# Optimization experiments

Hardware: AMD Instinct MI355X
Metric: run time of the kernel (lower is better)

Reference implementation:

```python
import jax, jax.numpy as jnp
import numpy as np

N_ATOMS, N_NBH, N_IN, N_FILTERS, N_OUT, N_GAUSS = 10000, 48, 128, 128, 128, 25
R_CUTOFF = 5.0
LOG2 = float(np.log(2.0))


def ssp(v):
    # shifted softplus, the SchNet activation
    return jax.nn.softplus(v) - LOG2


def setup_inputs() -> dict:
    key = jax.random.key(0)
    ks = jax.random.split(key, 10)
    x = jax.random.normal(ks[0], (N_ATOMS, N_IN), dtype=jnp.float32)
    dR = jax.random.uniform(ks[1], (N_ATOMS, N_NBH), dtype=jnp.float32) * 10.0  # distances in [0,10)
    dR_expanded = jax.random.normal(ks[2], (N_ATOMS, N_NBH, N_GAUSS), dtype=jnp.float32)
    pairwise_mask = jnp.ones((N_ATOMS, N_NBH), dtype=jnp.float32)
    neighbors_idx = jax.random.randint(ks[3], (N_ATOMS, N_NBH), 0, N_ATOMS, dtype=jnp.int32)
    s = 1.0 / np.sqrt(N_FILTERS)
    W1 = jax.random.normal(ks[4], (N_GAUSS, N_FILTERS), dtype=jnp.float32) * (1.0 / np.sqrt(N_GAUSS))
    b1 = jnp.zeros((N_FILTERS,), dtype=jnp.float32)
    W2 = jax.random.normal(ks[5], (N_FILTERS, N_FILTERS), dtype=jnp.float32) * s
    b2 = jnp.zeros((N_FILTERS,), dtype=jnp.float32)
    W_in2f = jax.random.normal(ks[6], (N_IN, N_FILTERS), dtype=jnp.float32) * (1.0 / np.sqrt(N_IN))
    W_f2out = jax.random.normal(ks[7], (N_FILTERS, N_OUT), dtype=jnp.float32) * s
    b_f2out = jnp.zeros((N_OUT,), dtype=jnp.float32)
    return {"x": x, "dR": dR, "dR_expanded": dR_expanded, "pairwise_mask": pairwise_mask,
            "neighbors_idx": neighbors_idx, "W1": W1, "b1": b1, "W2": W2, "b2": b2,
            "W_in2f": W_in2f, "W_f2out": W_f2out, "b_f2out": b_f2out}


def reference(x, dR, dR_expanded, pairwise_mask, neighbors_idx,
              W1, b1, W2, b2, W_in2f, W_f2out, b_f2out):
    # FilterNetwork: Dense + ssp + Dense, on Gaussian-smeared distances -> [N, K, F]
    W = jnp.einsum('nkg,gf->nkf', dR_expanded, W1) + b1
    W = jnp.einsum('nkf,fh->nkh', ssp(W), W2) + b2
    # HardCutoff: 1 where within cutoff
    C = (dR <= R_CUTOFF).astype(W.dtype)           # [N, K]
    W = W * C[..., None]
    # in2f (no bias), gather neighbor features
    y = x @ W_in2f                                  # [N, F]
    y = jnp.take(y, neighbors_idx, axis=0)          # [N, K, F] (gather == take_along_axis path)
    # filter-weighted multiply + masked sum aggregation over neighbor axis
    y = y * W
    y = jnp.sum(y * pairwise_mask[..., None], axis=1)  # [N, F]
    # f2out: Linear + shifted softplus
    return ssp(y @ W_f2out + b_f2out)               # [N, n_out]
```

## Files before the change

### kernel.cpp

```cpp
#include <hip/hip_runtime.h>
#include <hip/hip_bf16.h>


#define NA 10000
#define NK 48
#define NF 128
#define AT 4
#define DREP 40
#define HP   136

typedef __bf16 bf16x8 __attribute__((ext_vector_type(8)));
typedef float  f32x4  __attribute__((ext_vector_type(4)));

__device__ __forceinline__ unsigned short f2bs(float x) {
    return __builtin_bit_cast(unsigned short, (__bf16)x);
}
__device__ __forceinline__ float bs2f(unsigned short u) {
    return (float)__builtin_bit_cast(__bf16, u);
}
__device__ __forceinline__ float sspf(float v) {
    return fmaxf(v, 0.0f) + __logf(1.0f + __expf(-fabsf(v))) - 0.69314718056f;
}

__global__ __launch_bounds__(256) void prep_weights(
    const float* __restrict__ W1,
    const float* __restrict__ W2,
    const float* __restrict__ Wi,
    unsigned short* __restrict__ wsb)
{
    int i = blockIdx.x * 256 + threadIdx.x;
    if (i < 4096) {
        int f = i >> 5, g = i & 31;
        wsb[i] = (g < 25) ? f2bs(W1[g * NF + f]) : (unsigned short)0;
    } else if (i < 20480) {
        int j = i - 4096; int h = j >> 7, k = j & 127;
        wsb[i] = f2bs(W2[k * NF + h]);
    } else if (i < 36864) {
        int j = i - 20480; int f = j >> 7, k = j & 127;
        wsb[i] = f2bs(Wi[k * NF + f]);
    }
}

__global__ __launch_bounds__(256) void in2f_mfma(
    const float* __restrict__ x,
    const unsigned short* __restrict__ WiT,
    unsigned short* __restrict__ yfeatb)
{
    const int tid = threadIdx.x;
    const int w = tid >> 6;
    const int lane = tid & 63;
    const int r = lane & 15;
    const int q = lane >> 4;
    const int nt0 = w * 2;
    const int m0 = blockIdx.x * 16;

    bf16x8 a[4];
    #pragma unroll
    for (int ks = 0; ks < 4; ++ks) {
        const float4* xp = (const float4*)(x + (size_t)(m0 + r) * NF + ks * 32 + q * 8);
        float4 v0 = xp[0], v1 = xp[1];
        a[ks][0]=(__bf16)v0.x; a[ks][1]=(__bf16)v0.y; a[ks][2]=(__bf16)v0.z; a[ks][3]=(__bf16)v0.w;
        a[ks][4]=(__bf16)v1.x; a[ks][5]=(__bf16)v1.y; a[ks][6]=(__bf16)v1.z; a[ks][7]=(__bf16)v1.w;
    }

    f32x4 acc[2];
    acc[0] = (f32x4){0.f,0.f,0.f,0.f};
    acc[1] = (f32x4){0.f,0.f,0.f,0.f};
    #pragma unroll
    for (int ks = 0; ks < 4; ++ks) {
        bf16x8 b0 = *(const bf16x8*)(WiT + ((nt0    ) * 16 + r) * NF + ks * 32 + q * 8);
        bf16x8 b1 = *(const bf16x8*)(WiT + ((nt0 + 1) * 16 + r) * NF + ks * 32 + q * 8);
        acc[0] = __builtin_amdgcn_mfma_f32_16x16x32_bf16(a[ks], b0, acc[0], 0, 0, 0);
        acc[1] = __builtin_amdgcn_mfma_f32_16x16x32_bf16(a[ks], b1, acc[1], 0, 0, 0);
    }
    #pragma unroll
    for (int t = 0; t < 2; ++t)
        #pragma unroll
        for (int reg = 0; reg < 4; ++reg)
            yfeatb[(size_t)(m0 + q * 4 + reg) * NF + (nt0 + t) * 16 + r] = f2bs(acc[t][reg]);
}

__global__ __launch_bounds__(256) void cfconv_mfma(
    const float* __restrict__ dR,
    const float* __restrict__ dRe,
    const float* __restrict__ mask,
    const int*   __restrict__ nbr,
    const float* __restrict__ b1,
    const float* __restrict__ b2,
    const float* __restrict__ Wf2o,
    const float* __restrict__ bf2o,
    const unsigned short* __restrict__ W1T,
    const unsigned short* __restrict__ W2T,
    const unsigned short* __restrict__ yfeatb,
    float* __restrict__ out)
{
    __shared__ __align__(16) unsigned short s_dre[NK * DREP];
    __shared__ __align__(16) unsigned short s_H[NK * HP];
    __shared__ __align__(16) float s_y4[AT][NF];
    __shared__ __align__(16) float s_part[AT][256];
    __shared__ float s_cm[NK];
    __shared__ int   s_nb[NK];

    const int tid = threadIdx.x;
    const int w = tid >> 6;
    const int lane = tid & 63;
    const int r = lane & 15;
    const int q = lane >> 4;
    const int nt0 = w * 2;
    const int n0 = blockIdx.x * AT;

    const float bias1a = b1[nt0 * 16 + r];
    const float bias1b = b1[nt0 * 16 + 16 + r];
    const float bias2a = b2[nt0 * 16 + r];
    const float bias2b = b2[nt0 * 16 + 16 + r];
    bf16x8 bfr0 = *(const bf16x8*)(W1T + ((nt0    ) * 16 + r) * 32 + q * 8);
    bf16x8 bfr1 = *(const bf16x8*)(W1T + ((nt0 + 1) * 16 + r) * 32 + q * 8);
    bf16x8 bw[2][4];
    #pragma unroll
    for (int t = 0; t < 2; ++t)
        #pragma unroll
        for (int ks = 0; ks < 4; ++ks)
            bw[t][ks] = *(const bf16x8*)(W2T + ((nt0 + t) * 16 + r) * NF + ks * 32 + q * 8);

    {
        unsigned int* z = (unsigned int*)s_dre;
        for (int i = tid; i < NK * DREP / 2; i += 256) z[i] = 0u;
    }
    __syncthreads();

    for (int a = 0; a < AT; ++a) {
        const int n = n0 + a;

        if (tid < NK) {
            float d = dR[n * NK + tid];
            float m = mask[n * NK + tid];
            s_cm[tid] = (d <= 5.0f) ? m : 0.0f;
            s_nb[tid] = nbr[n * NK + tid] * NF;
        }
        {
            const float* dre = dRe + (size_t)n * (NK * 25);
            #pragma unroll
            for (int i = tid; i < NK * 25; i += 256) {
                int k = i / 25;
                int g = i - k * 25;
                s_dre[k * DREP + g] = f2bs(dre[i]);
            }
        }
        __syncthreads();

        #pragma unroll
        for (int mt = 0; mt < 3; ++mt) {
            bf16x8 af = *(const bf16x8*)(&s_dre[(mt * 16 + r) * DREP + q * 8]);
            f32x4 zf = (f32x4){0.f,0.f,0.f,0.f};
            f32x4 h0 = __builtin_amdgcn_mfma_f32_16x16x32_bf16(af, bfr0, zf, 0, 0, 0);
            f32x4 h1 = __builtin_amdgcn_mfma_f32_16x16x32_bf16(af, bfr1, zf, 0, 0, 0);
            #pragma unroll
            for (int reg = 0; reg < 4; ++reg) {
                int k = mt * 16 + q * 4 + reg;
                s_H[k * HP + nt0 * 16 + r]      = f2bs(sspf(h0[reg] + bias1a));
                s_H[k * HP + nt0 * 16 + 16 + r] = f2bs(sspf(h1[reg] + bias1b));
            }
        }
        __syncthreads();

        f32x4 acc[3][2];
        #pragma unroll
        for (int mt = 0; mt < 3; ++mt) {
            acc[mt][0] = (f32x4){0.f,0.f,0.f,0.f};
            acc[mt][1] = (f32x4){0.f,0.f,0.f,0.f};
        }
        #pragma unroll
        for (int ks = 0; ks < 4; ++ks) {
            #pragma unroll
            for (int mt = 0; mt < 3; ++mt) {
                bf16x8 af = *(const bf16x8*)(&s_H[(mt * 16 + r) * HP + ks * 32 + q * 8]);
                acc[mt][0] = __builtin_amdgcn_mfma_f32_16x16x32_bf16(af, bw[0][ks], acc[mt][0], 0, 0, 0);
                acc[mt][1] = __builtin_amdgcn_mfma_f32_16x16x32_bf16(af, bw[1][ks], acc[mt][1], 0, 0, 0);
            }
        }

        float part0 = 0.f, part1 = 0.f;
        const int h0i = nt0 * 16 + r;
        #pragma unroll
        for (int mt = 0; mt < 3; ++mt) {
            #pragma unroll
            for (int reg = 0; reg < 4; ++reg) {
                int k = mt * 16 + q * 4 + reg;
                float cmk = s_cm[k];
                int base = s_nb[k];
                part0 = fmaf(cmk * (acc[mt][0][reg] + bias2a), bs2f(yfeatb[base + h0i]), part0);
                part1 = fmaf(cmk * (acc[mt][1][reg] + bias2b), bs2f(yfeatb[base + h0i + 16]), part1);
            }
        }
        part0 += __shfl_xor(part0, 16);
        part0 += __shfl_xor(part0, 32);
        part1 += __shfl_xor(part1, 16);
        part1 += __shfl_xor(part1, 32);
        if (q == 0) {
            s_y4[a][h0i] = part0;
            s_y4[a][h0i + 16] = part1;
        }
        __syncthreads();
    }

    {
        int f = tid & 127;
        int half = tid >> 7;
        float o0 = 0.f, o1 = 0.f, o2 = 0.f, o3 = 0.f;
        const float* wp = Wf2o + (size_t)(half * 64) * NF + f;
        const float* y0 = &s_y4[0][half * 64];
        const float* y1 = &s_y4[1][half * 64];
        const float* y2 = &s_y4[2][half * 64];
        const float* y3 = &s_y4[3][half * 64];
        #pragma unroll 8
        for (int i = 0; i < 64; ++i) {
            float wv = wp[(size_t)i * NF];
            o0 = fmaf(y0[i], wv, o0);
            o1 = fmaf(y1[i], wv, o1);
            o2 = fmaf(y2[i], wv, o2);
            o3 = fmaf(y3[i], wv, o3);
        }
        s_part[0][tid] = o0;
        s_part[1][tid] = o1;
        s_part[2][tid] = o2;
        s_part[3][tid] = o3;
    }
    __syncthreads();
    if (tid < NF) {
        float bo = bf2o[tid];
        #pragma unroll
        for (int a = 0; a < AT; ++a)
            out[(size_t)(n0 + a) * NF + tid] = sspf(s_part[a][tid] + s_part[a][tid + 128] + bo);
    }
}

extern "C" void kernel_launch(void* const* d_in, const int* in_sizes, int n_in,
                              void* d_out, int out_size, void* d_ws, size_t ws_size,
                              hipStream_t stream)
{
    const float* x    = (const float*)d_in[0];
    const float* dR   = (const float*)d_in[1];
    const float* dRe  = (const float*)d_in[2];
    const float* mask = (const float*)d_in[3];
    const int*   nbr  = (const int*)d_in[4];
    const float* W1   = (const float*)d_in[5];
    const float* b1   = (const float*)d_in[6];
    const float* W2   = (const float*)d_in[7];
    const float* b2   = (const float*)d_in[8];
    const float* Wi2f = (const float*)d_in[9];
    const float* Wf2o = (const float*)d_in[10];
    const float* bf2o = (const float*)d_in[11];
    float* out = (float*)d_out;

    unsigned short* wsb = (unsigned short*)d_ws;
    unsigned short* W1T    = wsb;
    unsigned short* W2T    = wsb + 4096;
    unsigned short* WiT    = wsb + 20480;
    unsigned short* yfeatb = wsb + 36864;

    prep_weights<<<144, 256, 0, stream>>>(W1, W2, Wi2f, wsb);
    in2f_mfma<<<625, 256, 0, stream>>>(x, WiT, yfeatb);
    cfconv_mfma<<<NA / AT, 256, 0, stream>>>(dR, dRe, mask, nbr, b1, b2, Wf2o, bf2o,
                                             W1T, W2T, yfeatb, out);
}
```

Baseline: 204.2 us.

## Compact neighbors by cutoff per atom, one atom per block, MFMA output layer

New measurement: 226.5 us. 11.0% more time.

```diff
diff --git a/kernel.cpp b/kernel.cpp
--- a/kernel.cpp
+++ b/kernel.cpp
@@ -5,7 +5,6 @@
 #define NA 10000
 #define NK 48
 #define NF 128
-#define AT 4
 #define DREP 40
 #define HP   136
 
@@ -26,6 +25,7 @@
     const float* __restrict__ W1,
     const float* __restrict__ W2,
     const float* __restrict__ Wi,
+    const float* __restrict__ Wf2o,
     unsigned short* __restrict__ wsb)
 {
     int i = blockIdx.x * 256 + threadIdx.x;
@@ -38,6 +38,9 @@
     } else if (i < 36864) {
         int j = i - 20480; int f = j >> 7, k = j & 127;
         wsb[i] = f2bs(Wi[k * NF + f]);
+    } else if (i < 53248) {
+        int j = i - 36864; int o = j >> 7, k = j & 127;
+        wsb[i] = f2bs(Wf2o[k * NF + o]);
     }
 }
 
@@ -63,21 +66,20 @@
         a[ks][4]=(__bf16)v1.x; a[ks][5]=(__bf16)v1.y; a[ks][6]=(__bf16)v1.z; a[ks][7]=(__bf16)v1.w;
     }
 
-    f32x4 acc[2];
-    acc[0] = (f32x4){0.f,0.f,0.f,0.f};
-    acc[1] = (f32x4){0.f,0.f,0.f,0.f};
+    f32x4 acc0 = (f32x4){0.f,0.f,0.f,0.f};
+    f32x4 acc1 = (f32x4){0.f,0.f,0.f,0.f};
     #pragma unroll
     for (int ks = 0; ks < 4; ++ks) {
         bf16x8 b0 = *(const bf16x8*)(WiT + ((nt0    ) * 16 + r) * NF + ks * 32 + q * 8);
         bf16x8 b1 = *(const bf16x8*)(WiT + ((nt0 + 1) * 16 + r) * NF + ks * 32 + q * 8);
-        acc[0] = __builtin_amdgcn_mfma_f32_16x16x32_bf16(a[ks], b0, acc[0], 0, 0, 0);
-        acc[1] = __builtin_amdgcn_mfma_f32_16x16x32_bf16(a[ks], b1, acc[1], 0, 0, 0);
-    }
-    #pragma unroll
-    for (int t = 0; t < 2; ++t)
-        #pragma unroll
-        for (int reg = 0; reg < 4; ++reg)
-            yfeatb[(size_t)(m0 + q * 4 + reg) * NF + (nt0 + t) * 16 + r] = f2bs(acc[t][reg]);
+        acc0 = __builtin_amdgcn_mfma_f32_16x16x32_bf16(a[ks], b0, acc0, 0, 0, 0);
+        acc1 = __builtin_amdgcn_mfma_f32_16x16x32_bf16(a[ks], b1, acc1, 0, 0, 0);
+    }
+    #pragma unroll
+    for (int reg = 0; reg < 4; ++reg) {
+        yfeatb[(size_t)(m0 + q * 4 + reg) * NF + (nt0    ) * 16 + r] = f2bs(acc0[reg]);
+        yfeatb[(size_t)(m0 + q * 4 + reg) * NF + (nt0 + 1) * 16 + r] = f2bs(acc1[reg]);
+    }
 }
 
 __global__ __launch_bounds__(256) void cfconv_mfma(
@@ -87,32 +89,58 @@
     const int*   __restrict__ nbr,
     const float* __restrict__ b1,
     const float* __restrict__ b2,
-    const float* __restrict__ Wf2o,
     const float* __restrict__ bf2o,
     const unsigned short* __restrict__ W1T,
     const unsigned short* __restrict__ W2T,
+    const unsigned short* __restrict__ Wf2oT,
     const unsigned short* __restrict__ yfeatb,
     float* __restrict__ out)
 {
     __shared__ __align__(16) unsigned short s_dre[NK * DREP];
-    __shared__ __align__(16) unsigned short s_H[NK * HP];
-    __shared__ __align__(16) float s_y4[AT][NF];
-    __shared__ __align__(16) float s_part[AT][256];
+    __shared__ __align__(16) unsigned short s_Hc[16 * HP];
+    __shared__ __align__(16) unsigned short s_ybh[NF];
+    __shared__ __align__(16) unsigned short s_ybl[NF];
+    __shared__ __align__(16) float s_cmc[NK];
+    __shared__ __align__(16) int   s_nbc[NK];
     __shared__ float s_cm[NK];
     __shared__ int   s_nb[NK];
+    __shared__ int   s_ci[NK];
+    __shared__ int   s_kc;
 
     const int tid = threadIdx.x;
+    const int n = blockIdx.x;
     const int w = tid >> 6;
     const int lane = tid & 63;
     const int r = lane & 15;
     const int q = lane >> 4;
     const int nt0 = w * 2;
-    const int n0 = blockIdx.x * AT;
-
-    const float bias1a = b1[nt0 * 16 + r];
-    const float bias1b = b1[nt0 * 16 + 16 + r];
-    const float bias2a = b2[nt0 * 16 + r];
-    const float bias2b = b2[nt0 * 16 + 16 + r];
+    const int h0i = nt0 * 16 + r;
+
+    {
+        unsigned int* z = (unsigned int*)s_dre;
+        for (int i = tid; i < NK * DREP / 2; i += 256) z[i] = 0u;
+    }
+    if (tid < NK) {
+        float d = dR[n * NK + tid];
+        float m = mask[n * NK + tid];
+        s_cm[tid] = (d <= 5.0f) ? m : 0.0f;
+        s_nb[tid] = nbr[n * NK + tid] * NF;
+    }
+    __syncthreads();
+
+    if (tid == 0) {
+        int j = 0;
+        for (int k = 0; k < NK; ++k) {
+            float c = s_cm[k];
+            if (c != 0.0f) { s_ci[j] = k; s_cmc[j] = c; s_nbc[j] = s_nb[k]; ++j; }
+        }
+        s_kc = j;
+        for (int k = j; k < NK; ++k) { s_cmc[k] = 0.0f; s_nbc[k] = 0; }
+    }
+    const float bias1a = b1[h0i];
+    const float bias1b = b1[h0i + 16];
+    const float bias2a = b2[h0i];
+    const float bias2b = b2[h0i + 16];
     bf16x8 bfr0 = *(const bf16x8*)(W1T + ((nt0    ) * 16 + r) * 32 + q * 8);
     bf16x8 bfr1 = *(const bf16x8*)(W1T + ((nt0 + 1) * 16 + r) * 32 + q * 8);
     bf16x8 bw[2][4];
@@ -121,116 +149,98 @@
         #pragma unroll
         for (int ks = 0; ks < 4; ++ks)
             bw[t][ks] = *(const bf16x8*)(W2T + ((nt0 + t) * 16 + r) * NF + ks * 32 + q * 8);
+    __syncthreads();
+
+    const int kc = s_kc;
+    const int mtiles = (kc + 15) >> 4;
 
     {
-        unsigned int* z = (unsigned int*)s_dre;
-        for (int i = tid; i < NK * DREP / 2; i += 256) z[i] = 0u;
-    }
-    __syncthreads();
-
-    for (int a = 0; a < AT; ++a) {
-        const int n = n0 + a;
-
-        if (tid < NK) {
-            float d = dR[n * NK + tid];
-            float m = mask[n * NK + tid];
-            s_cm[tid] = (d <= 5.0f) ? m : 0.0f;
-            s_nb[tid] = nbr[n * NK + tid] * NF;
-        }
-        {
-            const float* dre = dRe + (size_t)n * (NK * 25);
+        const float* dre = dRe + (size_t)n * (NK * 25);
+        int tot = kc * 25;
+        for (int i = tid; i < tot; i += 256) {
+            int kidx = (int)((unsigned)i / 25u);
+            int g = i - kidx * 25;
+            s_dre[kidx * DREP + g] = f2bs(dre[s_ci[kidx] * 25 + g]);
+        }
+    }
+    __syncthreads();
+
+    float part0 = 0.f, part1 = 0.f;
+    for (int mt = 0; mt < mtiles; ++mt) {
+        const float* cmp = &s_cmc[mt * 16 + q * 4];
+        const int*   nbp = &s_nbc[mt * 16 + q * 4];
+        float cm0 = cmp[0], cm1 = cmp[1], cm2 = cmp[2], cm3 = cmp[3];
+
+        bf16x8 af = *(const bf16x8*)(&s_dre[(mt * 16 + r) * DREP + q * 8]);
+        f32x4 h0 = __builtin_amdgcn_mfma_f32_16x16x32_bf16(
+            af, bfr0, (f32x4){bias1a, bias1a, bias1a, bias1a}, 0, 0, 0);
+        f32x4 h1 = __builtin_amdgcn_mfma_f32_16x16x32_bf16(
+            af, bfr1, (f32x4){bias1b, bias1b, bias1b, bias1b}, 0, 0, 0);
+        s_Hc[(q * 4 + 0) * HP + h0i]      = f2bs(sspf(h0[0]) * cm0);
+        s_Hc[(q * 4 + 1) * HP + h0i]      = f2bs(sspf(h0[1]) * cm1);
+        s_Hc[(q * 4 + 2) * HP + h0i]      = f2bs(sspf(h0[2]) * cm2);
+        s_Hc[(q * 4 + 3) * HP + h0i]      = f2bs(sspf(h0[3]) * cm3);
+        s_Hc[(q * 4 + 0) * HP + h0i + 16] = f2bs(sspf(h1[0]) * cm0);
+        s_Hc[(q * 4 + 1) * HP + h0i + 16] = f2bs(sspf(h1[1]) * cm1);
+        s_Hc[(q * 4 + 2) * HP + h0i + 16] = f2bs(sspf(h1[2]) * cm2);
+        s_Hc[(q * 4 + 3) * HP + h0i + 16] = f2bs(sspf(h1[3]) * cm3);
+        __syncthreads();
+
+        f32x4 acc0 = (f32x4){cm0 * bias2a, cm1 * bias2a, cm2 * bias2a, cm3 * bias2a};
+        f32x4 acc1 = (f32x4){cm0 * bias2b, cm1 * bias2b, cm2 * bias2b, cm3 * bias2b};
+        #pragma unroll
+        for (int ks = 0; ks < 4; ++ks) {
+            bf16x8 ah = *(const bf16x8*)(&s_Hc[r * HP + ks * 32 + q * 8]);
+            acc0 = __builtin_amdgcn_mfma_f32_16x16x32_bf16(ah, bw[0][ks], acc0, 0, 0, 0);
+            acc1 = __builtin_amdgcn_mfma_f32_16x16x32_bf16(ah, bw[1][ks], acc1, 0, 0, 0);
+        }
+
+        #pragma unroll
+        for (int reg = 0; reg < 4; ++reg) {
+            int base = nbp[reg];
+            part0 = fmaf(acc0[reg], bs2f(yfeatb[base + h0i]),      part0);
+            part1 = fmaf(acc1[reg], bs2f(yfeatb[base + h0i + 16]), part1);
+        }
+        __syncthreads();
+    }
+
+    part0 += __shfl_xor(part0, 16);
+    part0 += __shfl_xor(part0, 32);
+    part1 += __shfl_xor(part1, 16);
+    part1 += __shfl_xor(part1, 32);
+    if (q == 0) {
+        unsigned short hh0 = f2bs(part0);
+        unsigned short hh1 = f2bs(part1);
+        s_ybh[h0i]      = hh0;
+        s_ybl[h0i]      = f2bs(part0 - bs2f(hh0));
+        s_ybh[h0i + 16] = hh1;
+        s_ybl[h0i + 16] = f2bs(part1 - bs2f(hh1));
+    }
+    __syncthreads();
+
+    {
+        bf16x8 ybh[4], ybl[4];
+        #pragma unroll
+        for (int ks = 0; ks < 4; ++ks) {
+            ybh[ks] = *(const bf16x8*)(&s_ybh[ks * 32 + q * 8]);
+            ybl[ks] = *(const bf16x8*)(&s_ybl[ks * 32 + q * 8]);
+        }
+        #pragma unroll
+        for (int t = 0; t < 2; ++t) {
+            int mt = nt0 + t;
+            f32x4 acc = *(const f32x4*)(bf2o + mt * 16 + q * 4);
             #pragma unroll
-            for (int i = tid; i < NK * 25; i += 256) {
-                int k = i / 25;
-                int g = i - k * 25;
-                s_dre[k * DREP + g] = f2bs(dre[i]);
+            for (int ks = 0; ks < 4; ++ks) {
+                bf16x8 afw = *(const bf16x8*)(Wf2oT + (mt * 16 + r) * NF + ks * 32 + q * 8);
+                acc = __builtin_amdgcn_mfma_f32_16x16x32_bf16(afw, ybh[ks], acc, 0, 0, 0);
+                acc = __builtin_amdgcn_mfma_f32_16x16x32_bf16(afw, ybl[ks], acc, 0, 0, 0);
             }
-        }
-        __syncthreads();
-
-        #pragma unroll
-        for (int mt = 0; mt < 3; ++mt) {
-            bf16x8 af = *(const bf16x8*)(&s_dre[(mt * 16 + r) * DREP + q * 8]);
-            f32x4 zf = (f32x4){0.f,0.f,0.f,0.f};
-            f32x4 h0 = __builtin_amdgcn_mfma_f32_16x16x32_bf16(af, bfr0, zf, 0, 0, 0);
-            f32x4 h1 = __builtin_amdgcn_mfma_f32_16x16x32_bf16(af, bfr1, zf, 0, 0, 0);
-            #pragma unroll
-            for (int reg = 0; reg < 4; ++reg) {
-                int k = mt * 16 + q * 4 + reg;
-                s_H[k * HP + nt0 * 16 + r]      = f2bs(sspf(h0[reg] + bias1a));
-                s_H[k * HP + nt0 * 16 + 16 + r] = f2bs(sspf(h1[reg] + bias1b));
+            if (r == 0) {
+                #pragma unroll
+                for (int reg = 0; reg < 4; ++reg)
+                    out[(size_t)n * NF + mt * 16 + q * 4 + reg] = sspf(acc[reg]);
             }
         }
-        __syncthreads();
-
-        f32x4 acc[3][2];
-        #pragma unroll
-        for (int mt = 0; mt < 3; ++mt) {
-            acc[mt][0] = (f32x4){0.f,0.f,0.f,0.f};
-            acc[mt][1] = (f32x4){0.f,0.f,0.f,0.f};
-        }
-        #pragma unroll
-        for (int ks = 0; ks < 4; ++ks) {
-            #pragma unroll
-            for (int mt = 0; mt < 3; ++mt) {
-                bf16x8 af = *(const bf16x8*)(&s_H[(mt * 16 + r) * HP + ks * 32 + q * 8]);
-                acc[mt][0] = __builtin_amdgcn_mfma_f32_16x16x32_bf16(af, bw[0][ks], acc[mt][0], 0, 0, 0);
-                acc[mt][1] = __builtin_amdgcn_mfma_f32_16x16x32_bf16(af, bw[1][ks], acc[mt][1], 0, 0, 0);
-            }
-        }
-
-        float part0 = 0.f, part1 = 0.f;
-        const int h0i = nt0 * 16 + r;
-        #pragma unroll
-        for (int mt = 0; mt < 3; ++mt) {
-            #pragma unroll
-            for (int reg = 0; reg < 4; ++reg) {
-                int k = mt * 16 + q * 4 + reg;
-                float cmk = s_cm[k];
-                int base = s_nb[k];
-                part0 = fmaf(cmk * (acc[mt][0][reg] + bias2a), bs2f(yfeatb[base + h0i]), part0);
-                part1 = fmaf(cmk * (acc[mt][1][reg] + bias2b), bs2f(yfeatb[base + h0i + 16]), part1);
-            }
-        }
-        part0 += __shfl_xor(part0, 16);
-        part0 += __shfl_xor(part0, 32);
-        part1 += __shfl_xor(part1, 16);
-        part1 += __shfl_xor(part1, 32);
-        if (q == 0) {
-            s_y4[a][h0i] = part0;
-            s_y4[a][h0i + 16] = part1;
-        }
-        __syncthreads();
-    }
-
-    {
-        int f = tid & 127;
-        int half = tid >> 7;
-        float o0 = 0.f, o1 = 0.f, o2 = 0.f, o3 = 0.f;
-        const float* wp = Wf2o + (size_t)(half * 64) * NF + f;
-        const float* y0 = &s_y4[0][half * 64];
-        const float* y1 = &s_y4[1][half * 64];
-        const float* y2 = &s_y4[2][half * 64];
-        const float* y3 = &s_y4[3][half * 64];
-        #pragma unroll 8
-        for (int i = 0; i < 64; ++i) {
-            float wv = wp[(size_t)i * NF];
-            o0 = fmaf(y0[i], wv, o0);
-            o1 = fmaf(y1[i], wv, o1);
-            o2 = fmaf(y2[i], wv, o2);
-            o3 = fmaf(y3[i], wv, o3);
-        }
-        s_part[0][tid] = o0;
-        s_part[1][tid] = o1;
-        s_part[2][tid] = o2;
-        s_part[3][tid] = o3;
-    }
-    __syncthreads();
-    if (tid < NF) {
-        float bo = bf2o[tid];
-        #pragma unroll
-        for (int a = 0; a < AT; ++a)
-            out[(size_t)(n0 + a) * NF + tid] = sspf(s_part[a][tid] + s_part[a][tid + 128] + bo);
     }
 }
 
@@ -256,10 +266,11 @@
     unsigned short* W1T    = wsb;
     unsigned short* W2T    = wsb + 4096;
     unsigned short* WiT    = wsb + 20480;
-    unsigned short* yfeatb = wsb + 36864;
-
-    prep_weights<<<144, 256, 0, stream>>>(W1, W2, Wi2f, wsb);
+    unsigned short* Wf2oT  = wsb + 36864;
+    unsigned short* yfeatb = wsb + 53248;
+
+    prep_weights<<<208, 256, 0, stream>>>(W1, W2, Wi2f, Wf2o, wsb);
     in2f_mfma<<<625, 256, 0, stream>>>(x, WiT, yfeatb);
-    cfconv_mfma<<<NA / AT, 256, 0, stream>>>(dR, dRe, mask, nbr, b1, b2, Wf2o, bf2o,
-                                             W1T, W2T, yfeatb, out);
-}
+    cfconv_mfma<<<NA, 256, 0, stream>>>(dR, dRe, mask, nbr, b1, b2, bf2o,
+                                        W1T, W2T, Wf2oT, yfeatb, out);
+}
```
